# Kernel optimization log

Measured on AMD Instinct MI355X. Metric: run time of the kernel, lower is better.

Reference implementation:

```python
import jax, jax.numpy as jnp
import numpy as np

B, D, H, L, E, NL, P, IMG, NT = 32, 768, 8, 6, 8, 256, 16, 224, 10
G = IMG // P          # 14 patches per side
NP = G * G            # 196 patches
HD = D // H           # 96 head dim
TOPK = 2
KEEP = 0.25
EPS = 1e-5


def layer_norm(x, g, b):
    m = x.mean(-1, keepdims=True)
    v = ((x - m) ** 2).mean(-1, keepdims=True)
    return (x - m) / jnp.sqrt(v + EPS) * g + b


def mha(q, kv, in_w, in_b, out_w, out_b):
    # torch nn.MultiheadAttention: packed in_proj (3D, D), out_proj (D, D)
    wq, wk, wv = in_w[:D], in_w[D:2 * D], in_w[2 * D:]
    bq, bk, bv = in_b[:D], in_b[D:2 * D], in_b[2 * D:]

    def heads(x, w, b):
        y = x @ w.T + b                               # (B, S, D)
        return y.reshape(x.shape[0], x.shape[1], H, HD).transpose(0, 2, 1, 3)

    Q = heads(q, wq, bq)
    K = heads(kv, wk, bk)
    V = heads(kv, wv, bv)
    scores = jnp.einsum('bhqd,bhkd->bhqk', Q, K) / np.sqrt(HD).astype(np.float32)
    attn = jax.nn.softmax(scores, axis=-1)
    o = jnp.einsum('bhqk,bhkd->bhqd', attn, V)
    o = o.transpose(0, 2, 1, 3).reshape(q.shape[0], q.shape[1], D)
    return o @ out_w.T + out_b


def moe(x, rw, rb, w1, b1, w2, b2):
    # top-2 routing; renormalize the top-k weights with a second softmax
    Bq, S, _ = x.shape
    T = Bq * S
    xt = x.reshape(T, D)
    probs = jax.nn.softmax(xt @ rw.T + rb, axis=-1)       # (T, E)
    tw, ti = jax.lax.top_k(probs, TOPK)                   # (T, K)
    tw = jax.nn.softmax(tw, axis=-1)
    # combine weights per expert: (T, E), >0 only for the chosen experts
    combine = (jax.nn.one_hot(ti, E, dtype=x.dtype) * tw[..., None]).sum(axis=1)
    out = jnp.zeros_like(xt)
    for e in range(E):  # fixed small expert count
        h = jax.nn.gelu(xt @ w1[e].T + b1[e], approximate=False)
        out = out + (h @ w2[e].T + b2[e]) * combine[:, e:e + 1]
    return out.reshape(Bq, S, D)


def _forward(images, type_ids, mask_noise, conv_w, conv_b, pos_emb, type_emb,
             latents, ca_in_w, ca_in_b, ca_out_w, ca_out_b, ca_ln_g, ca_ln_b,
             sa_in_w, sa_in_b, sa_out_w, sa_out_b, ln1_g, ln1_b,
             router_w, router_b, e_w1, e_b1, e_w2, e_b2, ln2_g, ln2_b):
    b = images.shape[0]
    # non-overlapping conv patch embed == unfold + matmul
    xp = images.reshape(b, 3, G, P, G, P).transpose(0, 2, 4, 1, 3, 5)
    xp = xp.reshape(b, NP, 3 * P * P)
    patches = xp @ conv_w.reshape(D, -1).T + conv_b        # (B, NP, D)
    patches = patches + pos_emb + type_emb[type_ids][:, None, :]
    # random masking: keep n_visible patches chosen by argsort of noise
    n_visible = int(NP * KEEP)
    order = jnp.argsort(mask_noise, axis=1)
    visible_indices = order[:, :n_visible]
    masked_indices = order[:, n_visible:]
    visible = jnp.take_along_axis(patches, visible_indices[:, :, None], axis=1)
    # cross attention from latents to visible patches
    lat = jnp.broadcast_to(latents, (b, NL, D))
    lat = layer_norm(lat + mha(lat, visible, ca_in_w, ca_in_b, ca_out_w, ca_out_b),
                     ca_ln_g, ca_ln_b)
    for l in range(L):
        a = mha(lat, lat, sa_in_w[l], sa_in_b[l], sa_out_w[l], sa_out_b[l])
        lat = layer_norm(lat + a, ln1_g[l], ln1_b[l])
        m = moe(lat, router_w[l], router_b[l], e_w1[l], e_b1[l], e_w2[l], e_b2[l])
        lat = layer_norm(lat + m, ln2_g[l], ln2_b[l])
    return lat, visible_indices, masked_indices


def setup_inputs() -> dict:
    key = jax.random.key(0)
    ks = jax.random.split(key, 16)
    r = lambda k, shape, s=0.02: jax.random.normal(k, shape, dtype=jnp.float32) * s
    z = lambda shape: jnp.zeros(shape, jnp.float32)
    o = lambda shape: jnp.ones(shape, jnp.float32)
    inp = {}
    inp['images'] = jax.random.normal(ks[0], (B, 3, IMG, IMG), dtype=jnp.float32)
    inp['type_ids'] = jax.random.randint(ks[1], (B,), 0, NT)
    inp['mask_noise'] = jax.random.uniform(ks[2], (B, NP), dtype=jnp.float32)
    inp['conv_w'] = r(ks[3], (D, 3, P, P))
    inp['conv_b'] = z((D,))
    inp['pos_emb'] = r(ks[4], (1, NP, D), 1.0)
    inp['type_emb'] = r(ks[5], (NT, D), 1.0)
    inp['latents'] = r(ks[6], (NL, D), 1.0)
    inp['ca_in_w'] = r(ks[7], (3 * D, D)); inp['ca_in_b'] = z((3 * D,))
    inp['ca_out_w'] = r(ks[8], (D, D)); inp['ca_out_b'] = z((D,))
    inp['ca_ln_g'] = o((D,)); inp['ca_ln_b'] = z((D,))
    inp['sa_in_w'] = r(ks[9], (L, 3 * D, D)); inp['sa_in_b'] = z((L, 3 * D))
    inp['sa_out_w'] = r(ks[10], (L, D, D)); inp['sa_out_b'] = z((L, D))
    inp['ln1_g'] = o((L, D)); inp['ln1_b'] = z((L, D))
    inp['router_w'] = r(ks[11], (L, E, D)); inp['router_b'] = z((L, E))
    inp['e_w1'] = r(ks[12], (L, E, 2 * D, D)); inp['e_b1'] = z((L, E, 2 * D))
    inp['e_w2'] = r(ks[13], (L, E, D, 2 * D)); inp['e_b2'] = z((L, E, D))
    inp['ln2_g'] = o((L, D)); inp['ln2_b'] = z((L, D))
    return inp


def reference(images, type_ids, mask_noise, conv_w, conv_b, pos_emb, type_emb,
              latents, ca_in_w, ca_in_b, ca_out_w, ca_out_b, ca_ln_g, ca_ln_b,
              sa_in_w, sa_in_b, sa_out_w, sa_out_b, ln1_g, ln1_b,
              router_w, router_b, e_w1, e_b1, e_w2, e_b2, ln2_g, ln2_b):
    return _forward(images, type_ids, mask_noise, conv_w, conv_b, pos_emb,
                    type_emb, latents, ca_in_w, ca_in_b, ca_out_w, ca_out_b,
                    ca_ln_g, ca_ln_b, sa_in_w, sa_in_b, sa_out_w, sa_out_b,
                    ln1_g, ln1_b, router_w, router_b, e_w1, e_b1, e_w2, e_b2,
                    ln2_g, ln2_b)
```

## Files before the change

### kernel.cpp

```cpp
#include <hip/hip_runtime.h>

typedef unsigned short u16;
typedef unsigned int u32;
typedef __attribute__((ext_vector_type(8))) u16 u16x8;
typedef __attribute__((ext_vector_type(8))) __bf16 bf16x8;
typedef __attribute__((ext_vector_type(4))) float f32x4;

#define DEV static __device__ __forceinline__

DEV float b2f(u16 u){ unsigned int i = ((unsigned int)u)<<16; float f; __builtin_memcpy(&f,&i,4); return f; }
DEV u16 f2b(float f){ unsigned int x; __builtin_memcpy(&x,&f,4); x = x + 0x7fffu + ((x>>16)&1u); return (u16)(x>>16); }

DEV void gll16(const u16* g, u16* l){
    __builtin_amdgcn_global_load_lds(
        (const __attribute__((address_space(1))) u32*)(const void*)g,
        (__attribute__((address_space(3))) u32*)(void*)l, 16, 0, 0);
}

template<bool F32>
DEV u16x8 ld8(const void* base, long off){
    if constexpr (F32){
        const float* p = (const float*)base + off;
        float4 a = *(const float4*)p;
        float4 b = *(const float4*)(p+4);
        u16x8 r;
        r[0]=f2b(a.x); r[1]=f2b(a.y); r[2]=f2b(a.z); r[3]=f2b(a.w);
        r[4]=f2b(b.x); r[5]=f2b(b.y); r[6]=f2b(b.z); r[7]=f2b(b.w);
        return r;
    } else {
        return *(const u16x8*)((const u16*)base + off);
    }
}
template<bool F32>
DEV const void* vadd(const void* p, long elems){
    if constexpr (F32) return (const void*)((const float*)p + elems);
    else               return (const void*)((const u16*)p + elems);
}

#define LAT_ELEMS 6291456
#define NVIS 49
#define NMASK 147
#define T_TOK 8192
#define MOE_CAP 17408
#define MOE_HALF 8704
#define KOFF 6291456L
#define VOFF 12582912L

__global__ __launch_bounds__(256) void wconv(const float* __restrict__ src, u16* __restrict__ dst, long n)
{
    long i = ((long)blockIdx.x*256 + threadIdx.x)*8;
    if (i >= n) return;
    *(u16x8*)(dst + i) = ld8<true>(src, i);
}

__global__ __launch_bounds__(256) void argsort_k(const float* __restrict__ noise,
                                                 int* __restrict__ order,
                                                 float* __restrict__ dout,
                                                 u16* __restrict__ zbuf)
{
    __shared__ float vals[196];
    __shared__ int ord[196];
    int b = blockIdx.x, tid = threadIdx.x;
    if (b == 0 && tid < 128) zbuf[tid] = 0;
    if (tid < 196) vals[tid] = noise[b*196 + tid];
    __syncthreads();
    if (tid < 196){
        float vi = vals[tid]; int rank = 0;
        for (int j=0;j<196;j++){ float vj = vals[j]; rank += (vj < vi) || (vj == vi && j < tid); }
        ord[rank] = tid;
    }
    __syncthreads();
    if (tid < 196){
        int v = ord[tid];
        order[b*196 + tid] = v;
        if (tid < NVIS) dout[LAT_ELEMS + b*NVIS + tid] = (float)v;
        else            dout[LAT_ELEMS + 32*NVIS + b*NMASK + (tid - NVIS)] = (float)v;
    }
}

__global__ __launch_bounds__(256) void patch_gather(const float* __restrict__ images,
                                                    const int* __restrict__ order,
                                                    u16* __restrict__ Ap)
{
    int i = blockIdx.x*256 + threadIdx.x;
    int t = i/48, kc = i - t*48;
    if (t >= 1664) return;
    if (t >= 1568){
        u16x8 z{};
        *(u16x8*)(Ap + (long)t*768 + kc*16)     = z;
        *(u16x8*)(Ap + (long)t*768 + kc*16 + 8) = z;
        return;
    }
    int b = t/49, vi = t - b*49;
    int p = order[b*196 + vi];
    int c = kc >> 4, py = kc & 15;
    int gy = p/14, gx = p - gy*14;
    const float* src = images + (((long)(b*3 + c)*224 + gy*16 + py)*224 + gx*16);
    u16x8 o0 = ld8<true>(src, 0);
    u16x8 o1 = ld8<true>(src, 8);
    *(u16x8*)(Ap + (long)t*768 + kc*16)     = o0;
    *(u16x8*)(Ap + (long)t*768 + kc*16 + 8) = o1;
}

__global__ __launch_bounds__(256) void add_pos_type(u16* __restrict__ vis,
                                                    const int* __restrict__ order,
                                                    const int* __restrict__ type_ids,
                                                    const float* __restrict__ pos,
                                                    const float* __restrict__ temb)
{
    int i = blockIdx.x*256 + threadIdx.x;
    int t = i/96, dc = (i - t*96)*8;
    if (t >= 1568) return;
    int b = t/49, vi = t - b*49;
    int p = order[b*196 + vi], tb = type_ids[b];
    u16x8 a = *(u16x8*)(vis + (long)t*768 + dc);
    const float* pp = pos  + (long)p*768 + dc;
    const float* tt = temb + (long)tb*768 + dc;
    float4 p0 = *(const float4*)pp, p1 = *(const float4*)(pp+4);
    float4 t0 = *(const float4*)tt, t1 = *(const float4*)(tt+4);
    u16x8 o;
    o[0]=f2b(b2f(a[0])+p0.x+t0.x); o[1]=f2b(b2f(a[1])+p0.y+t0.y);
    o[2]=f2b(b2f(a[2])+p0.z+t0.z); o[3]=f2b(b2f(a[3])+p0.w+t0.w);
    o[4]=f2b(b2f(a[4])+p1.x+t1.x); o[5]=f2b(b2f(a[5])+p1.y+t1.y);
    o[6]=f2b(b2f(a[6])+p1.z+t1.z); o[7]=f2b(b2f(a[7])+p1.w+t1.w);
    *(u16x8*)(vis + (long)t*768 + dc) = o;
}

template<int BK, int MT, bool BIAS, bool GELU, int GRP, bool AF32, bool BF32, bool SWZ, bool GLL>
__global__ __launch_bounds__(256,4) void gemm_nt(
    const void* __restrict__ A, const void* __restrict__ B, const float* __restrict__ bias,
    u16* __restrict__ C,
    int M, int N, int K, int lda, int ldb, int ldc,
    float scale, int ZLO, int NB,
    long sAh, long sAl, long sBh, long sBl, long sCh, long sCl,
    const int* __restrict__ aoff, const int* __restrict__ tos, const u16* __restrict__ zbuf,
    int row_base, long sBE, long sBiasE)
{
    int bx = blockIdx.x, by = blockIdx.y;
    if (SWZ){
        int nx = gridDim.x, ny = gridDim.y;
        int nwg = nx*ny;
        int flat = by*nx + bx;
        int q = nwg >> 3, r = nwg & 7;
        int xcd = flat & 7, idx = flat >> 3;
        int wg = (xcd < r ? xcd*(q+1) : r*(q+1) + (xcd - r)*q) + idx;
        bx = wg % nx; by = wg / nx;
    }
    int z = blockIdx.z; int zh = z / ZLO, zl = z - zh*ZLO;
    const void* Ab = vadd<AF32>(A, zh*sAh + zl*sAl);
    const void* Bb = vadd<BF32>(B, zh*sBh + zl*sBl);
    u16* Cb = C + zh*sCh + zl*sCl;
    const float* biasb = bias;
    int row0 = by*MT, col0 = bx*128;
    int lim = 0;
    if (GRP == 1 || GRP == 2){
        lim = aoff[8];
        int g0 = row_base + row0;
        if (g0 >= lim) return;
        int e = 0;
        #pragma unroll
        for (int i=1;i<8;i++) if (g0 >= aoff[i]) e = i;
        Bb = vadd<BF32>(B, (long)e*sBE);
        if (BIAS) biasb = bias + (long)e*sBiasE;
    }
    constexpr int SP = GLL ? BK : BK + 8;
    constexpr int MR = MT/32;
    __shared__ __align__(16) u16 As[MT*SP];
    __shared__ __align__(16) u16 Bs[128*SP];
    int tid = threadIdx.x;
    int lane = tid & 63, wv = tid >> 6;
    int wr = (wv>>1)*(MT/2), wc = (wv&1)*64;
    f32x4 acc[MR][4];
    #pragma unroll
    for (int m=0;m<MR;m++){
        #pragma unroll
        for (int n=0;n<4;n++) acc[m][n] = f32x4{0.f,0.f,0.f,0.f};
    }
    constexpr int RPC = BK/8;
    constexpr int RPI = 64/RPC;
    constexpr int NJA = MT*RPC/256;
    constexpr int NJB = 128*RPC/256;
    constexpr int PER = 128*RPC/256;
    int tA[4];
    if (GRP == 1){
        #pragma unroll
        for (int j=0;j<NJA;j++){
            int r = wv*(MT/4) + j*RPI + (lane/RPC);
            tA[j] = tos[row_base + row0 + r];
        }
    }
    for (int k0=0; k0<K; k0+=BK){
        if constexpr (GLL){
            int ch = lane % RPC;
            #pragma unroll
            for (int j=0;j<NJA;j++){
                int r  = wv*(MT/4) + j*RPI + (lane/RPC);
                const u16* sa;
                if (GRP == 1){
                    int t = tA[j];
                    sa = (t >= 0) ? (const u16*)Ab + (long)t*lda + k0 + ch*8 : zbuf + ch*8;
                } else {
                    sa = (const u16*)Ab + (long)(row0+r)*lda + k0 + ch*8;
                }
                gll16(sa, As + (wv*(MT/4) + j*RPI)*BK);
            }
            #pragma unroll
            for (int j=0;j<NJB;j++){
                int r = wv*32 + j*RPI + (lane/RPC);
                const u16* sb = (col0 + r < NB) ? (const u16*)Bb + (long)(col0+r)*ldb + k0 + ch*8
                                                : zbuf + ch*8;
                gll16(sb, Bs + (wv*32 + j*RPI)*BK);
            }
        } else if constexpr (MT == 128){
            #pragma unroll
            for (int j=0;j<PER;j++){
                int c = j*256 + tid;
                int r = c / RPC, cc = (c - r*RPC)*8;
                u16x8 va{}, vb{};
                if (GRP == 1){
                    int t = tA[j];
                    if (t >= 0) va = ld8<AF32>(Ab, (long)t*lda + k0 + cc);
                } else {
                    va = ld8<AF32>(Ab, (long)(row0+r)*lda + k0 + cc);
                }
                if (col0 + r < NB) vb = ld8<BF32>(Bb, (long)(col0+r)*ldb + k0 + cc);
                *(u16x8*)(As + r*SP + cc) = va;
                *(u16x8*)(Bs + r*SP + cc) = vb;
            }
        }
        __syncthreads();
        #pragma unroll
        for (int kk=0; kk<BK/32; kk++){
            bf16x8 af[MR], bg[4];
            #pragma unroll
            for (int m=0;m<MR;m++)
                af[m] = *(const bf16x8*)(As + (wr + m*16 + (lane&15))*SP + kk*32 + (lane>>4)*8);
            #pragma unroll
            for (int n=0;n<4;n++)
                bg[n] = *(const bf16x8*)(Bs + (wc + n*16 + (lane&15))*SP + kk*32 + (lane>>4)*8);
            #pragma unroll
            for (int m=0;m<MR;m++){
                #pragma unroll
                for (int n=0;n<4;n++)
                    acc[m][n] = __builtin_amdgcn_mfma_f32_16x16x32_bf16(af[m], bg[n], acc[m][n], 0,0,0);
            }
        }
        __syncthreads();
    }
    #pragma unroll
    for (int m=0;m<MR;m++){
        int rbase = row0 + wr + m*16 + ((lane>>4)<<2);
        #pragma unroll
        for (int n=0;n<4;n++){
            int col = col0 + wc + n*16 + (lane&15);
            if (col < N){
                float bv = BIAS ? biasb[col] : 0.f;
                #pragma unroll
                for (int j=0;j<4;j++){
                    int row = rbase + j;
                    bool ok = (row < M);
                    if (GRP == 1 || GRP == 2) ok = ok && (row_base + row) < lim;
                    if (ok){
                        float v = acc[m][n][j]*scale + bv;
                        if (GELU) v = 0.5f*v*(1.f + erff(v*0.70710678118f));
                        u16 ov = f2b(v);
                        if (GRP == 3){
                            if (col < 768){
                                Cb[(long)row*768 + col] = ov;
                            } else if (col < 1536){
                                Cb[sBE + (long)row*768 + (col - 768)] = ov;
                            } else {
                                int c96 = col - 1536;
                                int h = c96/96, d = c96 - h*96;
                                Cb[sBiasE + ((long)((row>>8)*8 + h)*96 + d)*256 + (row & 255)] = ov;
                            }
                        } else if (GRP == 2){
                            Cb[(long)(row_base + row)*ldc + col] = ov;
                        } else {
                            Cb[(long)row*ldc + col] = ov;
                        }
                    }
                }
            }
        }
    }
}

__global__ __launch_bounds__(256,2) void scores_sm(const u16* __restrict__ Q,
                                                   const u16* __restrict__ K,
                                                   u16* __restrict__ S)
{
    __shared__ __align__(16) u16 As[128*32];
    __shared__ __align__(16) u16 Bs[256*32];
    int z = blockIdx.y;
    int b = z >> 3, h = z & 7;
    const u16* Ab = Q + (long)b*196608 + h*96 + (long)blockIdx.x*128*768;
    const u16* Bb = K + (long)b*196608 + h*96;
    int tid = threadIdx.x, lane = tid & 63, wv = tid >> 6;
    f32x4 acc[2][16];
    #pragma unroll
    for (int m=0;m<2;m++){
        #pragma unroll
        for (int n=0;n<16;n++) acc[m][n] = f32x4{0.f,0.f,0.f,0.f};
    }
    int ch = lane & 3, rr = lane >> 2;
    for (int k0=0;k0<96;k0+=32){
        #pragma unroll
        for (int j=0;j<2;j++){
            int r = wv*32 + j*16 + rr;
            gll16(Ab + (long)r*768 + k0 + ch*8, As + (wv*128 + j*64)*8);
        }
        #pragma unroll
        for (int j=0;j<4;j++){
            int r = wv*64 + j*16 + rr;
            gll16(Bb + (long)r*768 + k0 + ch*8, Bs + (wv*256 + j*64)*8);
        }
        __syncthreads();
        bf16x8 af[2];
        #pragma unroll
        for (int m=0;m<2;m++)
            af[m] = *(const bf16x8*)(As + (wv*32 + m*16 + (lane&15))*32 + (lane>>4)*8);
        #pragma unroll
        for (int n=0;n<16;n++){
            bf16x8 bg = *(const bf16x8*)(Bs + (n*16 + (lane&15))*32 + (lane>>4)*8);
            acc[0][n] = __builtin_amdgcn_mfma_f32_16x16x32_bf16(af[0], bg, acc[0][n], 0,0,0);
            acc[1][n] = __builtin_amdgcn_mfma_f32_16x16x32_bf16(af[1], bg, acc[1][n], 0,0,0);
        }
        __syncthreads();
    }
    const float SCL = 0.10206207f;
    u16* Sz = S + (long)z*65536 + (long)blockIdx.x*128*256;
    #pragma unroll
    for (int m=0;m<2;m++){
        #pragma unroll
        for (int j=0;j<4;j++){
            float mx = -1e30f;
            #pragma unroll
            for (int n=0;n<16;n++) mx = fmaxf(mx, acc[m][n][j]);
            #pragma unroll
            for (int off=8; off>=1; off>>=1) mx = fmaxf(mx, __shfl_xor(mx, off, 64));
            float ev[16]; float sum = 0.f;
            #pragma unroll
            for (int n=0;n<16;n++){ ev[n] = __expf((acc[m][n][j]-mx)*SCL); sum += ev[n]; }
            #pragma unroll
            for (int off=8; off>=1; off>>=1) sum += __shfl_xor(sum, off, 64);
            float inv = 1.f/sum;
            int row = wv*32 + m*16 + ((lane>>4)<<2) + j;
            #pragma unroll
            for (int n=0;n<16;n++) Sz[(long)row*256 + n*16 + (lane&15)] = f2b(ev[n]*inv);
        }
    }
}

__global__ __launch_bounds__(256) void ca_attn(const u16* __restrict__ Qc,
                                               const u16* __restrict__ KV,
                                               u16* __restrict__ attn_out)
{
    __shared__ float Sm[256*49];
    __shared__ u16 KVs[49*96];
    int b = blockIdx.x, h = blockIdx.y, q = threadIdx.x;
    for (int i=q; i<49*96; i+=256){ int k=i/96, d=i-k*96; KVs[i] = KV[(long)(b*49+k)*1536 + h*96 + d]; }
    __syncthreads();
    float qv[96];
    #pragma unroll
    for (int d=0;d<96;d++) qv[d] = b2f(Qc[(long)q*768 + h*96 + d]);
    for (int k=0;k<49;k++){
        float a = 0.f;
        #pragma unroll
        for (int d=0;d<96;d++) a += qv[d]*b2f(KVs[k*96+d]);
        Sm[q*49+k] = a*0.10206207f;
    }
    __syncthreads();
    for (int i=q; i<49*96; i+=256){ int k=i/96, d=i-k*96; KVs[i] = KV[(long)(b*49+k)*1536 + 768 + h*96 + d]; }
    float mx = -1e30f;
    for (int k=0;k<49;k++) mx = fmaxf(mx, Sm[q*49+k]);
    float sum = 0.f;
    for (int k=0;k<49;k++){ float e = __expf(Sm[q*49+k]-mx); Sm[q*49+k]=e; sum+=e; }
    float inv = 1.f/sum;
    __syncthreads();
    for (int d=0;d<96;d++){
        float a = 0.f;
        for (int k=0;k<49;k++) a += Sm[q*49+k]*b2f(KVs[k*96+d]);
        attn_out[(long)(b*256+q)*768 + h*96 + d] = f2b(a*inv);
    }
}

template<int MODE, bool ROUTE>
__global__ __launch_bounds__(256) void ln_k(
    const float* __restrict__ res, int resmod,
    const u16* __restrict__ add,
    const u16* __restrict__ OutE, const int* __restrict__ sot, const float2* __restrict__ w01,
    const float* __restrict__ g, const float* __restrict__ bb,
    const float* __restrict__ rw, const float* __restrict__ rb,
    int2* __restrict__ e01o, float2* __restrict__ w01o,
    float* __restrict__ out, u16* __restrict__ outb, int T)
{
    int wid = threadIdx.x >> 6, lane = threadIdx.x & 63;
    int t = blockIdx.x*4 + wid; if (t >= T) return;
    const float* rp = res + (long)(t % resmod)*768;
    float x[12];
    #pragma unroll
    for (int j=0;j<3;j++){
        float4 v = *(const float4*)(rp + j*256 + lane*4);
        x[j*4+0]=v.x; x[j*4+1]=v.y; x[j*4+2]=v.z; x[j*4+3]=v.w;
    }
    if (MODE == 0){
        const u16* ap = add + (long)t*768;
        #pragma unroll
        for (int j=0;j<3;j++){
            ushort4 v = *(const ushort4*)(ap + j*256 + lane*4);
            x[j*4+0]+=b2f(v.x); x[j*4+1]+=b2f(v.y); x[j*4+2]+=b2f(v.z); x[j*4+3]+=b2f(v.w);
        }
    } else {
        int s0 = sot[2*t], s1 = sot[2*t+1];
        float2 w = w01[t];
        const u16* p0 = OutE + (long)s0*768;
        const u16* p1 = OutE + (long)s1*768;
        #pragma unroll
        for (int j=0;j<3;j++){
            ushort4 v0 = *(const ushort4*)(p0 + j*256 + lane*4);
            ushort4 v1 = *(const ushort4*)(p1 + j*256 + lane*4);
            x[j*4+0] += w.x*b2f(v0.x) + w.y*b2f(v1.x);
            x[j*4+1] += w.x*b2f(v0.y) + w.y*b2f(v1.y);
            x[j*4+2] += w.x*b2f(v0.z) + w.y*b2f(v1.z);
            x[j*4+3] += w.x*b2f(v0.w) + w.y*b2f(v1.w);
        }
    }
    float s = 0.f;
    #pragma unroll
    for (int i=0;i<12;i++) s += x[i];
    #pragma unroll
    for (int off=32; off>=1; off>>=1) s += __shfl_xor(s, off, 64);
    float m = s*(1.f/768.f);
    float s2 = 0.f;
    #pragma unroll
    for (int i=0;i<12;i++){ float d = x[i]-m; s2 += d*d; }
    #pragma unroll
    for (int off=32; off>=1; off>>=1) s2 += __shfl_xor(s2, off, 64);
    float rstd = rsqrtf(s2*(1.f/768.f) + 1e-5f);
    float y[12];
    #pragma unroll
    for (int j=0;j<3;j++){
        int col = j*256 + lane*4;
        float4 gg = *(const float4*)(g + col);
        float4 bv = *(const float4*)(bb + col);
        y[j*4+0] = (x[j*4+0]-m)*rstd*gg.x + bv.x;
        y[j*4+1] = (x[j*4+1]-m)*rstd*gg.y + bv.y;
        y[j*4+2] = (x[j*4+2]-m)*rstd*gg.z + bv.z;
        y[j*4+3] = (x[j*4+3]-m)*rstd*gg.w + bv.w;
        float4 o; o.x=y[j*4+0]; o.y=y[j*4+1]; o.z=y[j*4+2]; o.w=y[j*4+3];
        *(float4*)(out + (long)t*768 + col) = o;
        if (outb != nullptr){
            ushort4 ob;
            ob.x = f2b(o.x); ob.y = f2b(o.y); ob.z = f2b(o.z); ob.w = f2b(o.w);
            *(ushort4*)(outb + (long)t*768 + col) = ob;
        }
    }
    if (ROUTE){
        float part[8];
        #pragma unroll
        for (int e=0;e<8;e++){
            const float* wp = rw + e*768;
            float a = 0.f;
            #pragma unroll
            for (int j=0;j<3;j++){
                float4 w4 = *(const float4*)(wp + j*256 + lane*4);
                a += y[j*4+0]*w4.x + y[j*4+1]*w4.y + y[j*4+2]*w4.z + y[j*4+3]*w4.w;
            }
            part[e] = a;
        }
        #pragma unroll
        for (int e=0;e<8;e++){
            #pragma unroll
            for (int off=32; off>=1; off>>=1) part[e] += __shfl_xor(part[e], off, 64);
        }
        if (lane == 0){
            float pe[8];
            float mx = -1e30f;
            #pragma unroll
            for (int e=0;e<8;e++){ pe[e] = part[e] + rb[e]; mx = fmaxf(mx, pe[e]); }
            float sum = 0.f;
            #pragma unroll
            for (int e=0;e<8;e++){ pe[e] = __expf(pe[e]-mx); sum += pe[e]; }
            float inv = 1.f/sum;
            #pragma unroll
            for (int e=0;e<8;e++) pe[e] *= inv;
            int i0 = 0;
            #pragma unroll
            for (int e=1;e<8;e++) if (pe[e] > pe[i0]) i0 = e;
            int i1 = -1;
            for (int e=0;e<8;e++){ if (e == i0) continue; if (i1 < 0 || pe[e] > pe[i1]) i1 = e; }
            float ex = __expf(pe[i1] - pe[i0]);
            float w0 = 1.f/(1.f+ex), w1 = ex/(1.f+ex);
            e01o[t] = int2{i0, i1};
            w01o[t] = float2{w0, w1};
        }
    }
}

__global__ __launch_bounds__(256) void route_build(const int2* __restrict__ e01,
                                                   int* __restrict__ aoff_g,
                                                   int* __restrict__ tos, int* __restrict__ sot,
                                                   u16* __restrict__ zbuf)
{
    __shared__ int wsum[8][4];
    __shared__ int wbase[8][4];
    __shared__ int aoff_s[9];
    int tid = threadIdx.x, lane = tid & 63, wid = tid >> 6;
    for (int s = tid; s < MOE_CAP; s += 256) tos[s] = -1;
    if (tid < 128) zbuf[tid] = 0;
    int t0 = tid * 32;
    int lc[8];
    #pragma unroll
    for (int e=0;e<8;e++) lc[e] = 0;
    for (int i=0;i<32;i++){
        int2 e = e01[t0+i];
        lc[e.x]++; lc[e.y]++;
    }
    int excl[8];
    #pragma unroll
    for (int e=0;e<8;e++){
        int sc = lc[e];
        #pragma unroll
        for (int off=1; off<64; off<<=1){
            int n = __shfl_up(sc, off, 64);
            if (lane >= off) sc += n;
        }
        excl[e] = sc - lc[e];
        if (lane == 63) wsum[e][wid] = sc;
    }
    __syncthreads();
    if (tid == 0){
        int tot = 0;
        #pragma unroll
        for (int e=0;e<8;e++){
            int s = 0;
            #pragma unroll
            for (int w=0;w<4;w++){ wbase[e][w] = s; s += wsum[e][w]; }
            aoff_s[e] = tot;
            tot += (s + 127) & ~127;
        }
        aoff_s[8] = tot;
        #pragma unroll
        for (int e=0;e<9;e++) aoff_g[e] = aoff_s[e];
    }
    __syncthreads();
    int cur[8];
    #pragma unroll
    for (int e=0;e<8;e++) cur[e] = aoff_s[e] + wbase[e][wid] + excl[e];
    for (int i=0;i<32;i++){
        int t = t0 + i;
        int2 e = e01[t];
        int s0 = cur[e.x]++;
        tos[s0] = t; sot[2*t]   = s0;
        int s1 = cur[e.y]++;
        tos[s1] = t; sot[2*t+1] = s1;
    }
}

extern "C" void kernel_launch(void* const* d_in, const int* in_sizes, int n_in,
                              void* d_out, int out_size, void* d_ws, size_t ws_size,
                              hipStream_t stream)
{
    (void)in_sizes; (void)n_in; (void)out_size;
    const float* images   = (const float*)d_in[0];
    const int*   type_ids = (const int*)d_in[1];
    const float* noise    = (const float*)d_in[2];
    const float* conv_w   = (const float*)d_in[3];
    const float* conv_b   = (const float*)d_in[4];
    const float* pos_emb  = (const float*)d_in[5];
    const float* type_emb = (const float*)d_in[6];
    const float* latents  = (const float*)d_in[7];
    const float* ca_in_w  = (const float*)d_in[8];
    const float* ca_in_b  = (const float*)d_in[9];
    const float* ca_out_w = (const float*)d_in[10];
    const float* ca_out_b = (const float*)d_in[11];
    const float* ca_ln_g  = (const float*)d_in[12];
    const float* ca_ln_b  = (const float*)d_in[13];
    const float* sa_in_w  = (const float*)d_in[14];
    const float* sa_in_b  = (const float*)d_in[15];
    const float* sa_out_w = (const float*)d_in[16];
    const float* sa_out_b = (const float*)d_in[17];
    const float* ln1_g    = (const float*)d_in[18];
    const float* ln1_b    = (const float*)d_in[19];
    const float* router_w = (const float*)d_in[20];
    const float* router_b = (const float*)d_in[21];
    const float* e_w1     = (const float*)d_in[22];
    const float* e_b1     = (const float*)d_in[23];
    const float* e_w2     = (const float*)d_in[24];
    const float* e_b2     = (const float*)d_in[25];
    const float* ln2_g    = (const float*)d_in[26];
    const float* ln2_b    = (const float*)d_in[27];
    float* dout = (float*)d_out;
    float* lat  = dout;

    char* p = (char*)d_ws;
    auto alloc = [&](size_t n)->char*{ char* r = p; p += (n + 255) & ~(size_t)255; return r; };
    int*    order  = (int*)   alloc(32*196*4);
    int2*   e01    = (int2*)  alloc((size_t)T_TOK*8);
    float2* w01    = (float2*)alloc((size_t)T_TOK*8);
    int*    aoff   = (int*)   alloc(64);
    int*    tos    = (int*)   alloc((size_t)MOE_CAP*4);
    int*    sot    = (int*)   alloc((size_t)T_TOK*2*4);
    u16*    zbuf   = (u16*)   alloc(256);
    size_t aux_used = (size_t)(p - (char*)d_ws);
    const size_t WB_BYTES = 92798976ull + 260702208ull;
    bool wb  = ws_size >= aux_used + WB_BYTES;
    bool big = wb || ws_size >= aux_used + 92798976ull;
    u16* ar = (u16*)alloc(wb ? WB_BYTES : (big ? 92798976ull : 71303168ull));
    u16* latb   = big ? ar : nullptr;
    u16* common = big ? ar + 6291456 : ar;
    u16* wbufA  = wb ? ar + 6291456 + 40108032 : nullptr;
    u16* Ap  = common;
    u16* vis = common + 1277952;
    u16* KV  = common + 2555904;
    u16* Qc  = common + 5111808;
    u16* caO = common + 5308416;
    u16* caM = common + 11599872;
    u16* Qb  = common;
    u16* Vt  = common + VOFF;
    u16* S   = common + 18874368;
    u16* aO  = common;
    u16* mha = common + KOFF;
    u16* Hbuf = common;
    u16* OutE = common + (big ? 26738688 : 13369344);
    u16* cwb      = wbufA;
    u16* cainb    = wbufA + 589824;
    u16* caoutb   = wbufA + 2359296;
    u16* winbAll  = wbufA + 2949120;
    u16* woutbAll = wbufA + 13565952;
    u16* w1bAll   = wbufA + 17104896;
    u16* w2bAll   = wbufA + 73728000;

    const float ONE = 1.0f;
    const long Z0 = 0;

    argsort_k<<<32, 256, 0, stream>>>(noise, order, dout, zbuf);
    patch_gather<<<312, 256, 0, stream>>>(images, order, Ap);
    if (wb){
        wconv<<<288, 256, 0, stream>>>(conv_w, cwb, 589824);
        wconv<<<864, 256, 0, stream>>>(ca_in_w, cainb, 1769472);
        wconv<<<288, 256, 0, stream>>>(ca_out_w, caoutb, 589824);
        wconv<<<5184, 256, 0, stream>>>(sa_in_w, winbAll, 10616832);
        wconv<<<1728, 256, 0, stream>>>(sa_out_w, woutbAll, 3538944);
        wconv<<<27648, 256, 0, stream>>>(e_w1, w1bAll, 56623104);
        wconv<<<27648, 256, 0, stream>>>(e_w2, w2bAll, 56623104);
        gemm_nt<64,64,true,false,0,false,false,true,true><<<dim3(6,26,1),256,0,stream>>>(Ap, cwb, conv_b, vis,
            1664,768,768, 768,768,768, ONE, 1, 768, Z0,Z0,Z0,Z0,Z0,Z0, nullptr,nullptr,zbuf,0, Z0,Z0);
        add_pos_type<<<588, 256, 0, stream>>>(vis, order, type_ids, pos_emb, type_emb);
        gemm_nt<64,128,true,false,0,true,false,true,false><<<dim3(6,2,1),256,0,stream>>>(latents, cainb, ca_in_b, Qc,
            256,768,768, 768,768,768, ONE, 1, 768, Z0,Z0,Z0,Z0,Z0,Z0, nullptr,nullptr,zbuf,0, Z0,Z0);
        gemm_nt<64,64,true,false,0,false,false,true,true><<<dim3(12,26,1),256,0,stream>>>(vis, cainb + 589824, ca_in_b + 768, KV,
            1664,1536,768, 768,768,1536, ONE, 1, 1536, Z0,Z0,Z0,Z0,Z0,Z0, nullptr,nullptr,zbuf,0, Z0,Z0);
        ca_attn<<<dim3(32,8), 256, 0, stream>>>(Qc, KV, caO);
        gemm_nt<64,64,true,false,0,false,false,true,true><<<dim3(6,128,1),256,0,stream>>>(caO, caoutb, ca_out_b, caM,
            T_TOK,768,768, 768,768,768, ONE, 1, 768, Z0,Z0,Z0,Z0,Z0,Z0, nullptr,nullptr,zbuf,0, Z0,Z0);
    } else {
        gemm_nt<64,128,true,false,0,false,true,false,false><<<dim3(6,13,1),256,0,stream>>>(Ap, conv_w, conv_b, vis,
            1664,768,768, 768,768,768, ONE, 1, 768, Z0,Z0,Z0,Z0,Z0,Z0, nullptr,nullptr,zbuf,0, Z0,Z0);
        add_pos_type<<<588, 256, 0, stream>>>(vis, order, type_ids, pos_emb, type_emb);
        gemm_nt<64,128,true,false,0,true,true,false,false><<<dim3(6,2,1),256,0,stream>>>(latents, ca_in_w, ca_in_b, Qc,
            256,768,768, 768,768,768, ONE, 1, 768, Z0,Z0,Z0,Z0,Z0,Z0, nullptr,nullptr,zbuf,0, Z0,Z0);
        gemm_nt<64,128,true,false,0,false,true,false,false><<<dim3(12,13,1),256,0,stream>>>(vis, ca_in_w + 768*768, ca_in_b + 768, KV,
            1664,1536,768, 768,768,1536, ONE, 1, 1536, Z0,Z0,Z0,Z0,Z0,Z0, nullptr,nullptr,zbuf,0, Z0,Z0);
        ca_attn<<<dim3(32,8), 256, 0, stream>>>(Qc, KV, caO);
        gemm_nt<64,128,true,false,0,false,true,false,false><<<dim3(6,64,1),256,0,stream>>>(caO, ca_out_w, ca_out_b, caM,
            T_TOK,768,768, 768,768,768, ONE, 1, 768, Z0,Z0,Z0,Z0,Z0,Z0, nullptr,nullptr,zbuf,0, Z0,Z0);
    }
    ln_k<0,false><<<2048, 256, 0, stream>>>(latents, 256, caM, nullptr,nullptr,nullptr, ca_ln_g, ca_ln_b,
        nullptr,nullptr,nullptr,nullptr, lat, latb, T_TOK);

    for (int l=0; l<6; l++){
        const float* b_in  = sa_in_b  + l*2304;
        const float* b_out = sa_out_b + l*768;
        const float* b1 = e_b1 + l*8*1536;
        const float* b2 = e_b2 + l*8*768;
        const float* rwl = router_w + l*8*768;
        const float* rbl = router_b + l*8;
        if (wb){
            const u16* winb  = winbAll  + (long)l*1769472;
            const u16* woutb = woutbAll + (long)l*589824;
            const u16* w1b   = w1bAll   + (long)l*9437184;
            const u16* w2b   = w2bAll   + (long)l*9437184;
            gemm_nt<64,128,true,false,3,false,false,true,true><<<dim3(18,64,1),256,0,stream>>>(latb, winb, b_in, Qb,
                T_TOK,2304,768, 768,768,0, ONE, 1, 2304, Z0,Z0,Z0,Z0,Z0,Z0, nullptr,nullptr,zbuf,0, KOFF, VOFF);
            scores_sm<<<dim3(2,256), 256, 0, stream>>>(Qb, Qb + KOFF, S);
            gemm_nt<64,64,false,false,0,false,false,false,true><<<dim3(1,4,256),256,0,stream>>>(S, Vt, nullptr, aO,
                256,96,256, 256,256,768, ONE, 8, 96, 524288,65536, 196608,24576, 196608,96, nullptr,nullptr,zbuf,0, Z0,Z0);
            gemm_nt<64,64,true,false,0,false,false,true,true><<<dim3(6,128,1),256,0,stream>>>(aO, woutb, b_out, mha,
                T_TOK,768,768, 768,768,768, ONE, 1, 768, Z0,Z0,Z0,Z0,Z0,Z0, nullptr,nullptr,zbuf,0, Z0,Z0);
            ln_k<0,true><<<2048, 256, 0, stream>>>(lat, T_TOK, mha, nullptr,nullptr,nullptr, ln1_g + l*768, ln1_b + l*768,
                rwl, rbl, e01, w01, lat, latb, T_TOK);
            route_build<<<1, 256, 0, stream>>>(e01, aoff, tos, sot, zbuf);
            gemm_nt<64,128,true,true,1,false,false,true,true><<<dim3(12,136,1),256,0,stream>>>(latb, w1b, b1, Hbuf,
                MOE_CAP,1536,768, 768,768,1536, ONE, 1, 1536, Z0,Z0,Z0,Z0,Z0,Z0,
                aoff, tos, zbuf, 0, (long)1536*768, 1536);
            gemm_nt<64,128,true,false,2,false,false,true,true><<<dim3(6,136,1),256,0,stream>>>(Hbuf, w2b, b2, OutE,
                MOE_CAP,768,1536, 1536,1536,768, ONE, 1, 768, Z0,Z0,Z0,Z0,Z0,Z0,
                aoff, tos, zbuf, 0, (long)768*1536, 768);
            ln_k<1,false><<<2048, 256, 0, stream>>>(lat, T_TOK, nullptr, OutE, sot, w01, ln2_g + l*768, ln2_b + l*768,
                nullptr,nullptr,nullptr,nullptr, lat, latb, T_TOK);
        } else {
            const float* w_in  = sa_in_w  + (long)l*2304*768;
            const float* w_out = sa_out_w + (long)l*768*768;
            const float* w1 = e_w1 + (long)l*8*1536*768;
            const float* w2 = e_w2 + (long)l*8*768*1536;
            if (big){
                gemm_nt<64,128,true,false,3,false,true,false,false><<<dim3(18,64,1),256,0,stream>>>(latb, w_in, b_in, Qb,
                    T_TOK,2304,768, 768,768,0, ONE, 1, 2304, Z0,Z0,Z0,Z0,Z0,Z0, nullptr,nullptr,zbuf,0, KOFF, VOFF);
            } else {
                gemm_nt<64,128,true,false,3,true,true,false,false><<<dim3(18,64,1),256,0,stream>>>(lat, w_in, b_in, Qb,
                    T_TOK,2304,768, 768,768,0, ONE, 1, 2304, Z0,Z0,Z0,Z0,Z0,Z0, nullptr,nullptr,zbuf,0, KOFF, VOFF);
            }
            scores_sm<<<dim3(2,256), 256, 0, stream>>>(Qb, Qb + KOFF, S);
            gemm_nt<64,128,false,false,0,false,false,false,false><<<dim3(1,2,256),256,0,stream>>>(S, Vt, nullptr, aO,
                256,96,256, 256,256,768, ONE, 8, 96, 524288,65536, 196608,24576, 196608,96, nullptr,nullptr,zbuf,0, Z0,Z0);
            gemm_nt<64,128,true,false,0,false,true,false,false><<<dim3(6,64,1),256,0,stream>>>(aO, w_out, b_out, mha,
                T_TOK,768,768, 768,768,768, ONE, 1, 768, Z0,Z0,Z0,Z0,Z0,Z0, nullptr,nullptr,zbuf,0, Z0,Z0);
            ln_k<0,true><<<2048, 256, 0, stream>>>(lat, T_TOK, mha, nullptr,nullptr,nullptr, ln1_g + l*768, ln1_b + l*768,
                rwl, rbl, e01, w01, lat, latb, T_TOK);
            route_build<<<1, 256, 0, stream>>>(e01, aoff, tos, sot, zbuf);
            if (big){
                gemm_nt<64,128,true,true,1,false,true,false,false><<<dim3(12,136,1),256,0,stream>>>(latb, w1, b1, Hbuf,
                    MOE_CAP,1536,768, 768,768,1536, ONE, 1, 1536, Z0,Z0,Z0,Z0,Z0,Z0,
                    aoff, tos, zbuf, 0, (long)1536*768, 1536);
                gemm_nt<64,128,true,false,2,false,true,false,false><<<dim3(6,136,1),256,0,stream>>>(Hbuf, w2, b2, OutE,
                    MOE_CAP,768,1536, 1536,1536,768, ONE, 1, 768, Z0,Z0,Z0,Z0,Z0,Z0,
                    aoff, tos, zbuf, 0, (long)768*1536, 768);
            } else {
                for (int rb2=0; rb2<MOE_CAP; rb2+=MOE_HALF){
                    gemm_nt<64,128,true,true,1,true,true,false,false><<<dim3(12,68,1),256,0,stream>>>(lat, w1, b1, Hbuf,
                        MOE_HALF,1536,768, 768,768,1536, ONE, 1, 1536, Z0,Z0,Z0,Z0,Z0,Z0,
                        aoff, tos, zbuf, rb2, (long)1536*768, 1536);
                    gemm_nt<64,128,true,false,2,false,true,false,false><<<dim3(6,68,1),256,0,stream>>>(Hbuf, w2, b2, OutE,
                        MOE_HALF,768,1536, 1536,1536,768, ONE, 1, 768, Z0,Z0,Z0,Z0,Z0,Z0,
                        aoff, tos, zbuf, rb2, (long)768*1536, 768);
                }
            }
            ln_k<1,false><<<2048, 256, 0, stream>>>(lat, T_TOK, nullptr, OutE, sot, w01, ln2_g + l*768, ln2_b + l*768,
                nullptr,nullptr,nullptr,nullptr, lat, latb, T_TOK);
        }
    }
}
```

Before: 2.341 ms.

## Shrink score tiles, vectorize transposed V stores, widen route_build to 1024 threads

The scores+softmax kernel now handles 64 query rows per block instead of 128. That halves accumulator registers, doubles the grid and raises the occupancy target. The QKV GEMM epilogue gets a dedicated path that drops per-element branching and writes the transposed V output as 4-wide vector stores. The single-block routing kernel uses 1024 threads with 8 tokens each instead of 256 with 32, shortening its serial scan. The trade-off is more K-tile reloads across the smaller score blocks and the removal of bounds checks in the QKV epilogue.

```diff
diff --git a/kernel.cpp b/kernel.cpp
--- a/kernel.cpp
+++ b/kernel.cpp
@@ -247,6 +247,33 @@
         }
         __syncthreads();
     }
+    if (GRP == 3){
+        #pragma unroll
+        for (int m=0;m<MR;m++){
+            int rbase = row0 + wr + m*16 + ((lane>>4)<<2);
+            #pragma unroll
+            for (int n=0;n<4;n++){
+                int col = col0 + wc + n*16 + (lane&15);
+                float bv = biasb[col];
+                if (col < 1536){
+                    u16* base = (col < 768) ? Cb : Cb + sBE - 768;
+                    #pragma unroll
+                    for (int j=0;j<4;j++)
+                        base[(long)(rbase+j)*768 + col] = f2b(acc[m][n][j]*scale + bv);
+                } else {
+                    int c96 = col - 1536;
+                    int h = c96/96, d = c96 - h*96;
+                    ushort4 o4;
+                    o4.x = f2b(acc[m][n][0]*scale + bv);
+                    o4.y = f2b(acc[m][n][1]*scale + bv);
+                    o4.z = f2b(acc[m][n][2]*scale + bv);
+                    o4.w = f2b(acc[m][n][3]*scale + bv);
+                    *(ushort4*)(Cb + sBiasE + ((long)((rbase>>8)*8 + h)*96 + d)*256 + (rbase & 255)) = o4;
+                }
+            }
+        }
+        return;
+    }
     #pragma unroll
     for (int m=0;m<MR;m++){
         int rbase = row0 + wr + m*16 + ((lane>>4)<<2);
@@ -264,17 +291,7 @@
                         float v = acc[m][n][j]*scale + bv;
                         if (GELU) v = 0.5f*v*(1.f + erff(v*0.70710678118f));
                         u16 ov = f2b(v);
-                        if (GRP == 3){
-                            if (col < 768){
-                                Cb[(long)row*768 + col] = ov;
-                            } else if (col < 1536){
-                                Cb[sBE + (long)row*768 + (col - 768)] = ov;
-                            } else {
-                                int c96 = col - 1536;
-                                int h = c96/96, d = c96 - h*96;
-                                Cb[sBiasE + ((long)((row>>8)*8 + h)*96 + d)*256 + (row & 255)] = ov;
-                            }
-                        } else if (GRP == 2){
+                        if (GRP == 2){
                             Cb[(long)(row_base + row)*ldc + col] = ov;
                         } else {
                             Cb[(long)row*ldc + col] = ov;
@@ -286,69 +303,53 @@
     }
 }
 
-__global__ __launch_bounds__(256,2) void scores_sm(const u16* __restrict__ Q,
+__global__ __launch_bounds__(256,4) void scores_sm(const u16* __restrict__ Q,
                                                    const u16* __restrict__ K,
                                                    u16* __restrict__ S)
 {
-    __shared__ __align__(16) u16 As[128*32];
+    __shared__ __align__(16) u16 As[64*32];
     __shared__ __align__(16) u16 Bs[256*32];
     int z = blockIdx.y;
     int b = z >> 3, h = z & 7;
-    const u16* Ab = Q + (long)b*196608 + h*96 + (long)blockIdx.x*128*768;
+    const u16* Ab = Q + (long)b*196608 + h*96 + (long)blockIdx.x*64*768;
     const u16* Bb = K + (long)b*196608 + h*96;
     int tid = threadIdx.x, lane = tid & 63, wv = tid >> 6;
-    f32x4 acc[2][16];
-    #pragma unroll
-    for (int m=0;m<2;m++){
-        #pragma unroll
-        for (int n=0;n<16;n++) acc[m][n] = f32x4{0.f,0.f,0.f,0.f};
-    }
+    f32x4 acc[16];
+    #pragma unroll
+    for (int n=0;n<16;n++) acc[n] = f32x4{0.f,0.f,0.f,0.f};
     int ch = lane & 3, rr = lane >> 2;
     for (int k0=0;k0<96;k0+=32){
-        #pragma unroll
-        for (int j=0;j<2;j++){
-            int r = wv*32 + j*16 + rr;
-            gll16(Ab + (long)r*768 + k0 + ch*8, As + (wv*128 + j*64)*8);
-        }
-        #pragma unroll
-        for (int j=0;j<4;j++){
-            int r = wv*64 + j*16 + rr;
-            gll16(Bb + (long)r*768 + k0 + ch*8, Bs + (wv*256 + j*64)*8);
-        }
+        gll16(Ab + (long)(wv*16 + rr)*768 + k0 + ch*8, As + (wv*16)*32);
+        #pragma unroll
+        for (int jj=0;jj<4;jj++)
+            gll16(Bb + (long)(wv*64 + jj*16 + rr)*768 + k0 + ch*8, Bs + (wv*64 + jj*16)*32);
         __syncthreads();
-        bf16x8 af[2];
-        #pragma unroll
-        for (int m=0;m<2;m++)
-            af[m] = *(const bf16x8*)(As + (wv*32 + m*16 + (lane&15))*32 + (lane>>4)*8);
+        bf16x8 af = *(const bf16x8*)(As + (wv*16 + (lane&15))*32 + (lane>>4)*8);
         #pragma unroll
         for (int n=0;n<16;n++){
             bf16x8 bg = *(const bf16x8*)(Bs + (n*16 + (lane&15))*32 + (lane>>4)*8);
-            acc[0][n] = __builtin_amdgcn_mfma_f32_16x16x32_bf16(af[0], bg, acc[0][n], 0,0,0);
-            acc[1][n] = __builtin_amdgcn_mfma_f32_16x16x32_bf16(af[1], bg, acc[1][n], 0,0,0);
+            acc[n] = __builtin_amdgcn_mfma_f32_16x16x32_bf16(af, bg, acc[n], 0,0,0);
         }
         __syncthreads();
     }
     const float SCL = 0.10206207f;
-    u16* Sz = S + (long)z*65536 + (long)blockIdx.x*128*256;
-    #pragma unroll
-    for (int m=0;m<2;m++){
-        #pragma unroll
-        for (int j=0;j<4;j++){
-            float mx = -1e30f;
-            #pragma unroll
-            for (int n=0;n<16;n++) mx = fmaxf(mx, acc[m][n][j]);
-            #pragma unroll
-            for (int off=8; off>=1; off>>=1) mx = fmaxf(mx, __shfl_xor(mx, off, 64));
-            float ev[16]; float sum = 0.f;
-            #pragma unroll
-            for (int n=0;n<16;n++){ ev[n] = __expf((acc[m][n][j]-mx)*SCL); sum += ev[n]; }
-            #pragma unroll
-            for (int off=8; off>=1; off>>=1) sum += __shfl_xor(sum, off, 64);
-            float inv = 1.f/sum;
-            int row = wv*32 + m*16 + ((lane>>4)<<2) + j;
-            #pragma unroll
-            for (int n=0;n<16;n++) Sz[(long)row*256 + n*16 + (lane&15)] = f2b(ev[n]*inv);
-        }
+    u16* Sz = S + (long)z*65536 + (long)blockIdx.x*64*256;
+    #pragma unroll
+    for (int j=0;j<4;j++){
+        float mx = -1e30f;
+        #pragma unroll
+        for (int n=0;n<16;n++) mx = fmaxf(mx, acc[n][j]);
+        #pragma unroll
+        for (int off=8; off>=1; off>>=1) mx = fmaxf(mx, __shfl_xor(mx, off, 64));
+        float ev[16]; float sum = 0.f;
+        #pragma unroll
+        for (int n=0;n<16;n++){ ev[n] = __expf((acc[n][j]-mx)*SCL); sum += ev[n]; }
+        #pragma unroll
+        for (int off=8; off>=1; off>>=1) sum += __shfl_xor(sum, off, 64);
+        float inv = 1.f/sum;
+        int row = wv*16 + ((lane>>4)<<2) + j;
+        #pragma unroll
+        for (int n=0;n<16;n++) Sz[(long)row*256 + n*16 + (lane&15)] = f2b(ev[n]*inv);
     }
 }
 
@@ -498,22 +499,23 @@
     }
 }
 
-__global__ __launch_bounds__(256) void route_build(const int2* __restrict__ e01,
-                                                   int* __restrict__ aoff_g,
-                                                   int* __restrict__ tos, int* __restrict__ sot,
-                                                   u16* __restrict__ zbuf)
-{
-    __shared__ int wsum[8][4];
-    __shared__ int wbase[8][4];
+__global__ __launch_bounds__(1024) void route_build(const int2* __restrict__ e01,
+                                                    int* __restrict__ aoff_g,
+                                                    int* __restrict__ tos, int* __restrict__ sot,
+                                                    u16* __restrict__ zbuf)
+{
+    __shared__ int wsum[8][16];
+    __shared__ int wbase[8][16];
     __shared__ int aoff_s[9];
     int tid = threadIdx.x, lane = tid & 63, wid = tid >> 6;
-    for (int s = tid; s < MOE_CAP; s += 256) tos[s] = -1;
+    for (int s = tid; s < MOE_CAP; s += 1024) tos[s] = -1;
     if (tid < 128) zbuf[tid] = 0;
-    int t0 = tid * 32;
+    int t0 = tid * 8;
     int lc[8];
     #pragma unroll
     for (int e=0;e<8;e++) lc[e] = 0;
-    for (int i=0;i<32;i++){
+    #pragma unroll
+    for (int i=0;i<8;i++){
         int2 e = e01[t0+i];
         lc[e.x]++; lc[e.y]++;
     }
@@ -536,7 +538,7 @@
         for (int e=0;e<8;e++){
             int s = 0;
             #pragma unroll
-            for (int w=0;w<4;w++){ wbase[e][w] = s; s += wsum[e][w]; }
+            for (int w=0;w<16;w++){ wbase[e][w] = s; s += wsum[e][w]; }
             aoff_s[e] = tot;
             tot += (s + 127) & ~127;
         }
@@ -548,7 +550,8 @@
     int cur[8];
     #pragma unroll
     for (int e=0;e<8;e++) cur[e] = aoff_s[e] + wbase[e][wid] + excl[e];
-    for (int i=0;i<32;i++){
+    #pragma unroll
+    for (int i=0;i<8;i++){
         int t = t0 + i;
         int2 e = e01[t];
         int s0 = cur[e.x]++;
@@ -684,14 +687,14 @@
             const u16* w2b   = w2bAll   + (long)l*9437184;
             gemm_nt<64,128,true,false,3,false,false,true,true><<<dim3(18,64,1),256,0,stream>>>(latb, winb, b_in, Qb,
                 T_TOK,2304,768, 768,768,0, ONE, 1, 2304, Z0,Z0,Z0,Z0,Z0,Z0, nullptr,nullptr,zbuf,0, KOFF, VOFF);
-            scores_sm<<<dim3(2,256), 256, 0, stream>>>(Qb, Qb + KOFF, S);
+            scores_sm<<<dim3(4,256), 256, 0, stream>>>(Qb, Qb + KOFF, S);
             gemm_nt<64,64,false,false,0,false,false,false,true><<<dim3(1,4,256),256,0,stream>>>(S, Vt, nullptr, aO,
                 256,96,256, 256,256,768, ONE, 8, 96, 524288,65536, 196608,24576, 196608,96, nullptr,nullptr,zbuf,0, Z0,Z0);
             gemm_nt<64,64,true,false,0,false,false,true,true><<<dim3(6,128,1),256,0,stream>>>(aO, woutb, b_out, mha,
                 T_TOK,768,768, 768,768,768, ONE, 1, 768, Z0,Z0,Z0,Z0,Z0,Z0, nullptr,nullptr,zbuf,0, Z0,Z0);
             ln_k<0,true><<<2048, 256, 0, stream>>>(lat, T_TOK, mha, nullptr,nullptr,nullptr, ln1_g + l*768, ln1_b + l*768,
                 rwl, rbl, e01, w01, lat, latb, T_TOK);
-            route_build<<<1, 256, 0, stream>>>(e01, aoff, tos, sot, zbuf);
+            route_build<<<1, 1024, 0, stream>>>(e01, aoff, tos, sot, zbuf);
             gemm_nt<64,128,true,true,1,false,false,true,true><<<dim3(12,136,1),256,0,stream>>>(latb, w1b, b1, Hbuf,
                 MOE_CAP,1536,768, 768,768,1536, ONE, 1, 1536, Z0,Z0,Z0,Z0,Z0,Z0,
                 aoff, tos, zbuf, 0, (long)1536*768, 1536);
@@ -712,14 +715,14 @@
                 gemm_nt<64,128,true,false,3,true,true,false,false><<<dim3(18,64,1),256,0,stream>>>(lat, w_in, b_in, Qb,
                     T_TOK,2304,768, 768,768,0, ONE, 1, 2304, Z0,Z0,Z0,Z0,Z0,Z0, nullptr,nullptr,zbuf,0, KOFF, VOFF);
             }
-            scores_sm<<<dim3(2,256), 256, 0, stream>>>(Qb, Qb + KOFF, S);
+            scores_sm<<<dim3(4,256), 256, 0, stream>>>(Qb, Qb + KOFF, S);
             gemm_nt<64,128,false,false,0,false,false,false,false><<<dim3(1,2,256),256,0,stream>>>(S, Vt, nullptr, aO,
                 256,96,256, 256,256,768, ONE, 8, 96, 524288,65536, 196608,24576, 196608,96, nullptr,nullptr,zbuf,0, Z0,Z0);
             gemm_nt<64,128,true,false,0,false,true,false,false><<<dim3(6,64,1),256,0,stream>>>(aO, w_out, b_out, mha,
                 T_TOK,768,768, 768,768,768, ONE, 1, 768, Z0,Z0,Z0,Z0,Z0,Z0, nullptr,nullptr,zbuf,0, Z0,Z0);
             ln_k<0,true><<<2048, 256, 0, stream>>>(lat, T_TOK, mha, nullptr,nullptr,nullptr, ln1_g + l*768, ln1_b + l*768,
                 rwl, rbl, e01, w01, lat, latb, T_TOK);
-            route_build<<<1, 256, 0, stream>>>(e01, aoff, tos, sot, zbuf);
+            route_build<<<1, 1024, 0, stream>>>(e01, aoff, tos, sot, zbuf);
             if (big){
                 gemm_nt<64,128,true,true,1,false,true,false,false><<<dim3(12,136,1),256,0,stream>>>(latb, w1, b1, Hbuf,
                     MOE_CAP,1536,768, 768,768,1536, ONE, 1, 1536, Z0,Z0,Z0,Z0,Z0,Z0,
```

New measurement: 2.220 ms. 1.05x faster.
